# Performance work log

Hardware: AMD Instinct MI355X
Metric: run time of the kernel (lower is better)

## Reference

```python
import jax, jax.numpy as jnp
import numpy as np

C = 19
D = 128
TAU_HARD = 0.2
EMA = 0.999
BETA = 0.7
TH_I, TH_F = 0.5, 0.85
TL_I, TL_F = 0.1, 0.3
EPS = 1e-7


def _l2norm(x, axis):
    n = jnp.linalg.norm(x, axis=axis, keepdims=True)
    return x / jnp.maximum(n, 1e-12)


def _flatten_feat(feat):
    # [B,D,Hf,Wf] -> [N,D]
    B, Dd, Hf, Wf = feat.shape
    return feat.transpose(0, 2, 3, 1).reshape(-1, Dd)


def _build_protos(feat, labels, weights=None):
    # single-pass segment reduce replacing the per-class python loop
    f = _flatten_feat(feat)
    seg = labels.reshape(-1)
    w = jnp.ones(seg.shape, f.dtype) if weights is None else weights.reshape(-1)
    wsum_f = jax.ops.segment_sum(w[:, None] * f, seg, num_segments=C)  # [C,D]
    wsum = jax.ops.segment_sum(w, seg, num_segments=C)                 # [C]
    cnt = jax.ops.segment_sum(jnp.ones_like(w), seg, num_segments=C)
    proto = wsum_f / (wsum[:, None] + EPS)
    return proto, cnt >= 1.0


def _hard_contrastive(feat, labels, mem, mem_init):
    f = _l2norm(_flatten_feat(feat), axis=1)          # [N,D]
    lab = labels.reshape(-1)
    valid = mem_init[lab].astype(f.dtype)
    logits = (f @ mem.T) / TAU_HARD                   # [N,C]
    ce = -jnp.take_along_axis(jax.nn.log_softmax(logits, axis=1), lab[:, None], axis=1)[:, 0]
    nv = jnp.sum(valid)
    return jnp.where(nv > 0, jnp.sum(ce * valid) / jnp.maximum(nv, 1.0), 0.0)


def _ce_map(logits, target):
    # per-pixel cross entropy, logits [B,C,H,W], target [B,H,W]
    ls = jax.nn.log_softmax(logits, axis=1)
    return -jnp.take_along_axis(ls, target[:, None], axis=1)[:, 0]


def setup_inputs() -> dict:
    key = jax.random.key(0)
    ks = jax.random.split(key, 9)
    B, Hf, Wf = 4, 128, 128
    H = W = 512
    f = lambda k: jax.random.normal(k, (B, D, Hf, Wf), jnp.float32)
    g = lambda k: jax.random.normal(k, (B, C, H, W), jnp.float32)
    return {
        "feat_l1": f(ks[0]), "feat_l2": f(ks[1]),
        "feat_u1": f(ks[2]), "feat_u2": f(ks[3]),
        "logits_l1": g(ks[4]), "logits_l2": g(ks[5]),
        "logits_u1": g(ks[6]), "logits_u2": g(ks[7]),
        "memory": jnp.zeros((C, D), jnp.float32),
        "gt_labels": jax.random.randint(ks[8], (B, H, W), 0, C),
        "memory_init": jnp.zeros((C,), bool),
        "cur_iter": 10000,
        "max_iter": 40000,
    }


def reference(feat_l1, feat_l2, feat_u1, feat_u2, logits_l1, logits_l2,
              logits_u1, logits_u2, memory, gt_labels, memory_init,
              cur_iter, max_iter):
    B, _, Hf, Wf = feat_l1.shape
    H, W = logits_u1.shape[2], logits_u1.shape[3]

    q_u1 = jax.nn.softmax(logits_u1, axis=1)
    q_u2 = jax.nn.softmax(logits_u2, axis=1)

    # reliability r_u [B,H,W]
    y1 = jnp.argmax(q_u1, axis=1)
    y2 = jnp.argmax(q_u2, axis=1)
    agree = (y1 == y2).astype(q_u1.dtype)
    conf = (jnp.max(q_u1, axis=1) + jnp.max(q_u2, axis=1)) / 2.0
    m = (q_u1 + q_u2) / 2.0
    logm = jnp.log(jnp.maximum(m, EPS))
    kl1 = jnp.sum(q_u1 * (jnp.log(jnp.maximum(q_u1, EPS)) - logm), axis=1)
    kl2 = jnp.sum(q_u2 * (jnp.log(jnp.maximum(q_u2, EPS)) - logm), axis=1)
    r_u = agree * conf * jnp.exp(-(kl1 + kl2) / 2.0)

    # cosine-annealed thresholds
    ratio = float(cur_iter) / max(int(max_iter), 1)
    tau_high = TH_F - (TH_F - TH_I) * np.cos(np.pi * ratio / 2)

    # UCPS (pseudo labels are argmax of logits == argmax of softmax)
    loss_ucps = jnp.mean(jax.lax.stop_gradient(r_u) * (_ce_map(logits_u1, y2) + _ce_map(logits_u2, y1)))

    # nearest downsample (integer stride, matches torch nearest floor indexing)
    ih = jnp.arange(Hf) * (H // Hf)
    iw = jnp.arange(Wf) * (W // Wf)
    gt_down = gt_labels[:, ih][:, :, iw]
    pseudo_consensus = jnp.where(y1 != y2, 0, y1)
    pseudo_u_down = pseudo_consensus[:, ih][:, :, iw]
    # bilinear (align_corners=False == half-pixel, no antialias)
    r_u_down = jax.image.resize(r_u, (B, Hf, Wf), method='linear', antialias=False)

    anchor_mask = r_u_down > tau_high

    feat_l = (feat_l1 + feat_l2) / 2.0
    feat_u = (feat_u1 + feat_u2) / 2.0
    pl, pl_pres = _build_protos(feat_l, gt_down)
    anchor_r = jnp.where(anchor_mask, r_u_down, 0.0)
    pu, pu_pres = _build_protos(feat_u, pseudo_u_down, anchor_r)

    both = pl_pres & pu_pres
    merged = jnp.where(both[:, None], BETA * pl + (1.0 - BETA) * pu,
                       jnp.where(pl_pres[:, None], pl, pu))
    present = pl_pres | pu_pres
    merged = jax.lax.stop_gradient(merged)  # update_memory is no_grad

    p_norm = _l2norm(merged, axis=1)
    ema = _l2norm(EMA * memory + (1.0 - EMA) * p_norm, axis=1)
    new_mem = jnp.where((present & ~memory_init)[:, None], p_norm,
                        jnp.where((present & memory_init)[:, None], ema, memory))
    new_init = memory_init | present
    new_mem = jax.lax.stop_gradient(new_mem)

    loss_hard_l = (_hard_contrastive(feat_l1, gt_down, new_mem, new_init)
                   + _hard_contrastive(feat_l2, gt_down, new_mem, new_init)) / 2.0
    # contrastive_mode == 'all_hard'
    loss_hard_u = (_hard_contrastive(feat_u1, pseudo_u_down, new_mem, new_init)
                   + _hard_contrastive(feat_u2, pseudo_u_down, new_mem, new_init)) / 2.0

    loss_dgpc = loss_hard_l + loss_hard_u  # loss_soft == 0 in all_hard mode
    return jnp.stack([loss_dgpc, loss_ucps])
```

## Files before the change

kernel.cpp:

```cpp
#include <hip/hip_runtime.h>
#include <math.h>

#define NCLS 19
#define DD   128
#define EPSV 1e-7f
#define LOGEPS -16.118095651f

#define OFF_TAU    0
#define OFF_CNTL   8
#define OFF_WSUMU  32
#define OFF_CNTU   64
#define OFF_CE     96
#define OFF_VALID  100
#define OFF_UCPS   104
#define OFF_SUML   128
#define OFF_SUMU   2560
#define OFF_MEM    4992
#define OFF_INIT   7424
#define OFF_RUD    7456
#define OFF_PSEUDO 72992
#define ZERO_N     72992

__device__ __forceinline__ void fatom(float* p, float v) { unsafeAtomicAdd(p, v); }

__global__ __launch_bounds__(256) void kZ(float* __restrict__ W,
                                          const int* __restrict__ cur_it,
                                          const int* __restrict__ max_it) {
    int i = blockIdx.x * 256 + threadIdx.x;
    if (i == 0) {
        int mi = max_it[0]; if (mi < 1) mi = 1;
        double ratio = (double)cur_it[0] / (double)mi;
        W[OFF_TAU] = (float)(0.85 - (0.85 - 0.5) * cos(M_PI * ratio * 0.5));
    } else if (i < ZERO_N) {
        W[i] = 0.0f;
    }
}

__global__ __launch_bounds__(256, 2) void kB(const float* __restrict__ lu1,
                                             const float* __restrict__ lu2,
                                             float* __restrict__ W) {
    float* rud = W + OFF_RUD;
    int* pseudo = (int*)(W + OFF_PSEUDO);
    int t = blockIdx.x * 256 + threadIdx.x;
    int b = t >> 16;
    int rem4 = (t << 2) & 262143;
    int h = rem4 >> 9, w0 = rem4 & 511;

    const float4* p1 = (const float4*)lu1 + (size_t)b * (NCLS * 65536) + (rem4 >> 2);
    const float4* p2 = (const float4*)lu2 + (size_t)b * (NCLS * 65536) + (rem4 >> 2);

    float4 v1[NCLS], v2[NCLS];
#pragma unroll
    for (int c = 0; c < NCLS; c++) v1[c] = p1[c * 65536];
#pragma unroll
    for (int c = 0; c < NCLS; c++) v2[c] = p2[c * 65536];
    const float* a1 = (const float*)v1;
    const float* a2 = (const float*)v2;

    float contrib = 0.f;
    float ru12 = 0.f;
    int pl0 = 0;

#pragma unroll
    for (int e = 0; e < 4; e++) {
        float m1 = a1[e]; int y1 = 0;
        float m2 = a2[e]; int y2 = 0;
#pragma unroll
        for (int c = 1; c < NCLS; c++) {
            float x1 = a1[c * 4 + e], x2 = a2[c * 4 + e];
            if (x1 > m1) { m1 = x1; y1 = c; }
            if (x2 > m2) { m2 = x2; y2 = c; }
        }
        float s1 = 0.f, s2 = 0.f;
#pragma unroll
        for (int c = 0; c < NCLS; c++) {
            s1 += __expf(a1[c * 4 + e] - m1);
            s2 += __expf(a2[c * 4 + e] - m2);
        }
        float lse1 = m1 + __logf(s1);
        float lse2 = m2 + __logf(s2);

        float kl = 0.f, l1y2 = a1[e], l2y1 = a2[e];
#pragma unroll
        for (int c = 0; c < NCLS; c++) {
            float x1 = a1[c * 4 + e], x2 = a2[c * 4 + e];
            float lq1 = x1 - lse1, lq2 = x2 - lse2;
            float q1 = __expf(lq1), q2 = __expf(lq2);
            float mm = 0.5f * (q1 + q2);
            float lm = __logf(fmaxf(mm, EPSV));
            kl += q1 * (fmaxf(lq1, LOGEPS) - lm) + q2 * (fmaxf(lq2, LOGEPS) - lm);
            if (c == y2) l1y2 = x1;
            if (c == y1) l2y1 = x2;
        }
        float conf = 0.5f * (1.f / s1 + 1.f / s2);
        float r_u = (y1 == y2) ? conf * __expf(-0.5f * kl) : 0.f;
        float ce = (lse1 - l1y2) + (lse2 - l2y1);
        contrib += r_u * ce;
        if (e == 1 || e == 2) ru12 += r_u;
        if (e == 0) pl0 = (y1 == y2) ? y1 : 0;
    }

    float cs = contrib;
#pragma unroll
    for (int o = 32; o > 0; o >>= 1) cs += __shfl_down(cs, o, 64);
    __shared__ float wsum[4];
    if ((threadIdx.x & 63) == 0) wsum[threadIdx.x >> 6] = cs;
    __syncthreads();
    if (threadIdx.x == 0) fatom(&W[OFF_UCPS], wsum[0] + wsum[1] + wsum[2] + wsum[3]);

    int hm = h & 3;
    int didx = b * 16384 + (h >> 2) * 128 + (w0 >> 2);
    if (hm == 1 || hm == 2) fatom(&rud[didx], 0.25f * ru12);
    if (hm == 0) pseudo[didx] = pl0;
}

__global__ __launch_bounds__(256) void kC(const float* __restrict__ fl1,
                                          const float* __restrict__ fl2,
                                          const float* __restrict__ fu1,
                                          const float* __restrict__ fu2,
                                          const int* __restrict__ gt,
                                          float* __restrict__ W) {
    __shared__ float tile[DD * 33];
    __shared__ float accL[2 * NCLS * DD];
    __shared__ int   sLab[32], sCu[32];
    __shared__ float sW[32];
    __shared__ float sCntL[NCLS], sCntU[NCLS], sWUs[NCLS];

    int tid = threadIdx.x;
    for (int i = tid; i < 2 * NCLS * DD; i += 256) accL[i] = 0.f;
    if (tid < NCLS) { sCntL[tid] = 0.f; sCntU[tid] = 0.f; sWUs[tid] = 0.f; }
    __syncthreads();

    int P0 = blockIdx.x * 128;
    int b = P0 >> 14;
    const float tau = W[OFF_TAU];
    const float* rud = W + OFF_RUD;
    const int* pseudo = (const int*)(W + OFF_PSEUDO);
    size_t gb = (size_t)b * 2097152;

    int d = tid & 127, pg = tid >> 7;

    for (int T = 0; T < 4; T++) {
        int rem0 = (P0 + T * 32) & 16383;
        if (tid < 32) {
            int rem = rem0 + tid;
            int bp = b * 16384 + rem;
            int ii = rem >> 7, jj = rem & 127;
            int cl = gt[b * 262144 + ii * 2048 + jj * 4];
            int cu = pseudo[bp];
            float rd = rud[bp];
            float w = (rd > tau) ? rd : 0.f;
            sLab[tid] = cl; sCu[tid] = cu; sW[tid] = w;
            fatom(&sCntL[cl], 1.f);
            fatom(&sCntU[cu], 1.f);
            if (w > 0.f) fatom(&sWUs[cu], w);
        }
        for (int i = tid; i < 1024; i += 256) {
            int dd = i >> 3, p4 = (i & 7) << 2;
            size_t g = gb + (size_t)dd * 16384 + rem0 + p4;
            float4 x1 = *(const float4*)(fl1 + g);
            float4 x2 = *(const float4*)(fl2 + g);
            float* tp = &tile[dd * 33 + p4];
            tp[0] = 0.5f * (x1.x + x2.x);
            tp[1] = 0.5f * (x1.y + x2.y);
            tp[2] = 0.5f * (x1.z + x2.z);
            tp[3] = 0.5f * (x1.w + x2.w);
        }
        __syncthreads();
        float* aL = &accL[pg * (NCLS * DD) + d];
#pragma unroll
        for (int p = pg * 16; p < pg * 16 + 16; p++) {
            int c = sLab[p];
            aL[c * DD] += tile[d * 33 + p];
            float w = sW[p];
            if (w > 0.f) {
                size_t g = gb + (size_t)d * 16384 + rem0 + p;
                fatom(&W[OFF_SUMU + sCu[p] * DD + d], w * 0.5f * (fu1[g] + fu2[g]));
            }
        }
        __syncthreads();
    }
    for (int i = tid; i < NCLS * DD; i += 256)
        fatom(&W[OFF_SUML + i], accL[i] + accL[NCLS * DD + i]);
    if (tid < NCLS) {
        fatom(&W[OFF_CNTL + tid], sCntL[tid]);
        fatom(&W[OFF_WSUMU + tid], sWUs[tid]);
        fatom(&W[OFF_CNTU + tid], sCntU[tid]);
    }
}

__global__ __launch_bounds__(128) void kD(const float* __restrict__ mem,
                                          const unsigned char* __restrict__ minit,
                                          float* __restrict__ W) {
    int c = blockIdx.x, d = threadIdx.x;
    __shared__ float red[128];
    float cntL = W[OFF_CNTL + c], wsU = W[OFF_WSUMU + c], cntU = W[OFF_CNTU + c];
    bool plp = cntL >= 1.f, pup = cntU >= 1.f;
    float pl = W[OFF_SUML + c * DD + d] / (cntL + EPSV);
    float pu = W[OFF_SUMU + c * DD + d] / (wsU + EPSV);
    float merged = (plp && pup) ? (0.7f * pl + 0.3f * pu) : (plp ? pl : pu);

    red[d] = merged * merged; __syncthreads();
    for (int s = 64; s > 0; s >>= 1) { if (d < s) red[d] += red[d + s]; __syncthreads(); }
    float nrm = red[0];
    __syncthreads();
    float pn = merged / fmaxf(sqrtf(nrm), 1e-12f);

    float mo = mem[c * DD + d];
    float e = 0.999f * mo + 0.001f * pn;
    red[d] = e * e; __syncthreads();
    for (int s = 64; s > 0; s >>= 1) { if (d < s) red[d] += red[d + s]; __syncthreads(); }
    float ne = red[0];
    float ema = e / fmaxf(sqrtf(ne), 1e-12f);

    bool present = plp || pup;
    bool init = (minit[c] != 0);
    float nm = present ? (init ? ema : pn) : mo;
    W[OFF_MEM + c * DD + d] = nm;
    if (d == 0) W[OFF_INIT + c] = (init || present) ? 1.f : 0.f;
}

__device__ __forceinline__ void pix_loss(const float dots[NCLS], float nn, int lab,
                                         const float* sInit, float& ce_acc, float& v_acc) {
    float inv = 5.0f / fmaxf(sqrtf(nn), 1e-12f);
    float lg[NCLS];
#pragma unroll
    for (int c = 0; c < NCLS; c++) lg[c] = dots[c] * inv;
    float mx = lg[0];
#pragma unroll
    for (int c = 1; c < NCLS; c++) mx = fmaxf(mx, lg[c]);
    float s = 0.f;
#pragma unroll
    for (int c = 0; c < NCLS; c++) s += __expf(lg[c] - mx);
    float lse = mx + __logf(s);
    float ll = lg[0];
#pragma unroll
    for (int c = 1; c < NCLS; c++) if (c == lab) ll = lg[c];
    float vld = sInit[lab];
    ce_acc += vld * (lse - ll);
    v_acc += vld;
}

__global__ __launch_bounds__(256) void kE(const float* __restrict__ f0,
                                          const float* __restrict__ f1,
                                          const float* __restrict__ f2,
                                          const float* __restrict__ f3,
                                          const int* __restrict__ gt,
                                          float* __restrict__ W) {
    __shared__ __align__(16) float sMem[NCLS * DD];
    __shared__ float sInit[NCLS];
    __shared__ float redA[256], redB[256];
    int fid = blockIdx.y;
    const float* feat = (fid == 0) ? f0 : (fid == 1) ? f1 : (fid == 2) ? f2 : f3;
    for (int i = threadIdx.x; i < NCLS * DD; i += 256) sMem[i] = W[OFF_MEM + i];
    if (threadIdx.x < NCLS) sInit[threadIdx.x] = W[OFF_INIT + threadIdx.x];
    __syncthreads();

    int p0 = blockIdx.x * 512 + threadIdx.x;
    int b = p0 >> 14;
    int rem0 = p0 & 16383;
    const float* fp = feat + (size_t)b * 2097152 + rem0;

    float dots0[NCLS], dots1[NCLS];
#pragma unroll
    for (int c = 0; c < NCLS; c++) { dots0[c] = 0.f; dots1[c] = 0.f; }
    float n0 = 0.f, n1 = 0.f;

    for (int d0 = 0; d0 < DD; d0 += 8) {
        const float* fpp = fp + (size_t)d0 * 16384;
        float a[8], bb[8];
#pragma unroll
        for (int j = 0; j < 8; j++) {
            a[j]  = fpp[(size_t)j * 16384];
            bb[j] = fpp[(size_t)j * 16384 + 256];
        }
#pragma unroll
        for (int j = 0; j < 8; j++) { n0 += a[j] * a[j]; n1 += bb[j] * bb[j]; }
#pragma unroll
        for (int c = 0; c < NCLS; c++) {
            float4 m0 = *(const float4*)&sMem[c * DD + d0];
            float4 m1 = *(const float4*)&sMem[c * DD + d0 + 4];
            dots0[c] += a[0] * m0.x + a[1] * m0.y + a[2] * m0.z + a[3] * m0.w
                      + a[4] * m1.x + a[5] * m1.y + a[6] * m1.z + a[7] * m1.w;
            dots1[c] += bb[0] * m0.x + bb[1] * m0.y + bb[2] * m0.z + bb[3] * m0.w
                      + bb[4] * m1.x + bb[5] * m1.y + bb[6] * m1.z + bb[7] * m1.w;
        }
    }

    const int* pseudo = (const int*)(W + OFF_PSEUDO);
    int rem1 = rem0 + 256;
    int lab0 = (fid < 2) ? gt[b * 262144 + (rem0 >> 7) * 2048 + (rem0 & 127) * 4] : pseudo[p0];
    int lab1 = (fid < 2) ? gt[b * 262144 + (rem1 >> 7) * 2048 + (rem1 & 127) * 4] : pseudo[p0 + 256];

    float ce_acc = 0.f, v_acc = 0.f;
    pix_loss(dots0, n0, lab0, sInit, ce_acc, v_acc);
    pix_loss(dots1, n1, lab1, sInit, ce_acc, v_acc);

    redA[threadIdx.x] = ce_acc;
    redB[threadIdx.x] = v_acc;
    __syncthreads();
    for (int s = 128; s > 0; s >>= 1) {
        if (threadIdx.x < s) { redA[threadIdx.x] += redA[threadIdx.x + s]; redB[threadIdx.x] += redB[threadIdx.x + s]; }
        __syncthreads();
    }
    if (threadIdx.x == 0) {
        fatom(&W[OFF_CE + fid], redA[0]);
        fatom(&W[OFF_VALID + fid], redB[0]);
    }
}

__global__ void kF(float* __restrict__ out, const float* __restrict__ W) {
    if (threadIdx.x == 0 && blockIdx.x == 0) {
        float h[4];
#pragma unroll
        for (int i = 0; i < 4; i++) {
            float nv = W[OFF_VALID + i];
            h[i] = (nv > 0.f) ? W[OFF_CE + i] / fmaxf(nv, 1.f) : 0.f;
        }
        out[0] = 0.5f * (h[0] + h[1]) + 0.5f * (h[2] + h[3]);
        out[1] = W[OFF_UCPS] * (1.0f / 1048576.0f);
    }
}

extern "C" void kernel_launch(void* const* d_in, const int* in_sizes, int n_in,
                              void* d_out, int out_size, void* d_ws, size_t ws_size,
                              hipStream_t stream) {
    const float* fl1 = (const float*)d_in[0];
    const float* fl2 = (const float*)d_in[1];
    const float* fu1 = (const float*)d_in[2];
    const float* fu2 = (const float*)d_in[3];
    const float* lu1 = (const float*)d_in[6];
    const float* lu2 = (const float*)d_in[7];
    const float* mem = (const float*)d_in[8];
    const int* gt = (const int*)d_in[9];
    const unsigned char* minit = (const unsigned char*)d_in[10];
    const int* cur = (const int*)d_in[11];
    const int* mxi = (const int*)d_in[12];
    float* W = (float*)d_ws;
    float* out = (float*)d_out;

    kZ<<<286, 256, 0, stream>>>(W, cur, mxi);
    kB<<<1024, 256, 0, stream>>>(lu1, lu2, W);
    kC<<<512, 256, 0, stream>>>(fl1, fl2, fu1, fu2, gt, W);
    kD<<<NCLS, 128, 0, stream>>>(mem, minit, W);
    kE<<<dim3(128, 4), 256, 0, stream>>>(fl1, fl2, fu1, fu2, gt, W);
    kF<<<1, 64, 0, stream>>>(out, W);
}
```

Baseline: 419.2 us.

## Compute the KL and CE terms only for pixels where the two argmaxes agree

The pseudo-label kernel now runs an argmax-only first pass, one image row per block with float2 loads. Pixels whose two argmaxes agree are compacted into shared memory, and only those run the logsumexp, KL and CE work, reading their logits a second time. Pixels that disagree contribute zero weight, so their transcendental work is skipped exactly. In exchange, surviving pixels reload their logits with scattered scalar loads, and the kernel adds shared-memory atomics and higher occupancy launch bounds.

```diff
diff --git a/kernel.cpp b/kernel.cpp
--- a/kernel.cpp
+++ b/kernel.cpp
@@ -36,82 +36,103 @@
     }
 }
 
-__global__ __launch_bounds__(256, 2) void kB(const float* __restrict__ lu1,
+__global__ __launch_bounds__(256, 6) void kB(const float* __restrict__ lu1,
                                              const float* __restrict__ lu2,
                                              float* __restrict__ W) {
+    __shared__ unsigned int sPk[512];
+    __shared__ float sM1[512], sM2[512];
+    __shared__ unsigned int sCnt;
+    __shared__ float sCE;
+
     float* rud = W + OFF_RUD;
     int* pseudo = (int*)(W + OFF_PSEUDO);
-    int t = blockIdx.x * 256 + threadIdx.x;
-    int b = t >> 16;
-    int rem4 = (t << 2) & 262143;
-    int h = rem4 >> 9, w0 = rem4 & 511;
-
-    const float4* p1 = (const float4*)lu1 + (size_t)b * (NCLS * 65536) + (rem4 >> 2);
-    const float4* p2 = (const float4*)lu2 + (size_t)b * (NCLS * 65536) + (rem4 >> 2);
-
-    float4 v1[NCLS], v2[NCLS];
-#pragma unroll
-    for (int c = 0; c < NCLS; c++) v1[c] = p1[c * 65536];
-#pragma unroll
-    for (int c = 0; c < NCLS; c++) v2[c] = p2[c * 65536];
-    const float* a1 = (const float*)v1;
-    const float* a2 = (const float*)v2;
-
-    float contrib = 0.f;
-    float ru12 = 0.f;
-    int pl0 = 0;
-
-#pragma unroll
-    for (int e = 0; e < 4; e++) {
-        float m1 = a1[e]; int y1 = 0;
-        float m2 = a2[e]; int y2 = 0;
-#pragma unroll
-        for (int c = 1; c < NCLS; c++) {
-            float x1 = a1[c * 4 + e], x2 = a2[c * 4 + e];
-            if (x1 > m1) { m1 = x1; y1 = c; }
-            if (x2 > m2) { m2 = x2; y2 = c; }
-        }
-        float s1 = 0.f, s2 = 0.f;
+
+    int blk = blockIdx.x;
+    int b = blk >> 9;
+    int h = blk & 511;
+    int t = threadIdx.x;
+    if (t == 0) { sCnt = 0u; sCE = 0.f; }
+    __syncthreads();
+
+    size_t base = (size_t)b * (NCLS * 262144) + (size_t)h * 512;
+    const float2* p1 = (const float2*)(lu1 + base) + t;
+    const float2* p2 = (const float2*)(lu2 + base) + t;
+
+    float m1a, m1b, m2a, m2b;
+    int y1a = 0, y1b = 0, y2a = 0, y2b = 0;
+    {
+        float2 x1 = p1[0], x2 = p2[0];
+        m1a = x1.x; m1b = x1.y; m2a = x2.x; m2b = x2.y;
+    }
+#pragma unroll
+    for (int c = 1; c < NCLS; c++) {
+        float2 x1 = p1[(size_t)c * 131072];
+        float2 x2 = p2[(size_t)c * 131072];
+        if (x1.x > m1a) { m1a = x1.x; y1a = c; }
+        if (x1.y > m1b) { m1b = x1.y; y1b = c; }
+        if (x2.x > m2a) { m2a = x2.x; y2a = c; }
+        if (x2.y > m2b) { m2b = x2.y; y2b = c; }
+    }
+
+    int wa = t << 1, wb = wa + 1;
+    bool aga = (y1a == y2a), agb = (y1b == y2b);
+
+    if ((h & 3) == 0 && (t & 1) == 0)
+        pseudo[b * 16384 + (h >> 2) * 128 + (wa >> 2)] = aga ? y1a : 0;
+
+    if (aga) {
+        unsigned int i = atomicAdd(&sCnt, 1u);
+        sPk[i] = ((unsigned)wa << 5) | (unsigned)y1a;
+        sM1[i] = m1a; sM2[i] = m2a;
+    }
+    if (agb) {
+        unsigned int i = atomicAdd(&sCnt, 1u);
+        sPk[i] = ((unsigned)wb << 5) | (unsigned)y1b;
+        sM1[i] = m1b; sM2[i] = m2b;
+    }
+    __syncthreads();
+
+    int n = (int)sCnt;
+    int hm = h & 3;
+    for (int i = t; i < n; i += 256) {
+        unsigned pk = sPk[i];
+        int w = (int)(pk >> 5), y = (int)(pk & 31u);
+        float m1 = sM1[i], m2 = sM2[i];
+        const float* q1 = lu1 + base + w;
+        const float* q2 = lu2 + base + w;
+
+        float s1 = 0.f, s2 = 0.f, l1y = 0.f, l2y = 0.f;
 #pragma unroll
         for (int c = 0; c < NCLS; c++) {
-            s1 += __expf(a1[c * 4 + e] - m1);
-            s2 += __expf(a2[c * 4 + e] - m2);
+            float x1 = q1[(size_t)c * 262144];
+            float x2 = q2[(size_t)c * 262144];
+            s1 += __expf(x1 - m1);
+            s2 += __expf(x2 - m2);
+            if (c == y) { l1y = x1; l2y = x2; }
         }
         float lse1 = m1 + __logf(s1);
         float lse2 = m2 + __logf(s2);
 
-        float kl = 0.f, l1y2 = a1[e], l2y1 = a2[e];
+        float kl = 0.f;
 #pragma unroll
         for (int c = 0; c < NCLS; c++) {
-            float x1 = a1[c * 4 + e], x2 = a2[c * 4 + e];
+            float x1 = q1[(size_t)c * 262144];
+            float x2 = q2[(size_t)c * 262144];
             float lq1 = x1 - lse1, lq2 = x2 - lse2;
-            float q1 = __expf(lq1), q2 = __expf(lq2);
-            float mm = 0.5f * (q1 + q2);
+            float e1 = __expf(lq1), e2 = __expf(lq2);
+            float mm = 0.5f * (e1 + e2);
             float lm = __logf(fmaxf(mm, EPSV));
-            kl += q1 * (fmaxf(lq1, LOGEPS) - lm) + q2 * (fmaxf(lq2, LOGEPS) - lm);
-            if (c == y2) l1y2 = x1;
-            if (c == y1) l2y1 = x2;
+            kl += e1 * (fmaxf(lq1, LOGEPS) - lm) + e2 * (fmaxf(lq2, LOGEPS) - lm);
         }
         float conf = 0.5f * (1.f / s1 + 1.f / s2);
-        float r_u = (y1 == y2) ? conf * __expf(-0.5f * kl) : 0.f;
-        float ce = (lse1 - l1y2) + (lse2 - l2y1);
-        contrib += r_u * ce;
-        if (e == 1 || e == 2) ru12 += r_u;
-        if (e == 0) pl0 = (y1 == y2) ? y1 : 0;
-    }
-
-    float cs = contrib;
-#pragma unroll
-    for (int o = 32; o > 0; o >>= 1) cs += __shfl_down(cs, o, 64);
-    __shared__ float wsum[4];
-    if ((threadIdx.x & 63) == 0) wsum[threadIdx.x >> 6] = cs;
-    __syncthreads();
-    if (threadIdx.x == 0) fatom(&W[OFF_UCPS], wsum[0] + wsum[1] + wsum[2] + wsum[3]);
-
-    int hm = h & 3;
-    int didx = b * 16384 + (h >> 2) * 128 + (w0 >> 2);
-    if (hm == 1 || hm == 2) fatom(&rud[didx], 0.25f * ru12);
-    if (hm == 0) pseudo[didx] = pl0;
+        float r_u = conf * __expf(-0.5f * kl);
+        float ce = (lse1 - l1y) + (lse2 - l2y);
+        fatom(&sCE, r_u * ce);
+        if ((hm == 1 || hm == 2) && ((w & 3) == 1 || (w & 3) == 2))
+            fatom(&rud[b * 16384 + (h >> 2) * 128 + (w >> 2)], 0.25f * r_u);
+    }
+    __syncthreads();
+    if (t == 0) fatom(&W[OFF_UCPS], sCE);
 }
 
 __global__ __launch_bounds__(256) void kC(const float* __restrict__ fl1,
@@ -340,7 +361,7 @@
     float* out = (float*)d_out;
 
     kZ<<<286, 256, 0, stream>>>(W, cur, mxi);
-    kB<<<1024, 256, 0, stream>>>(lu1, lu2, W);
+    kB<<<2048, 256, 0, stream>>>(lu1, lu2, W);
     kC<<<512, 256, 0, stream>>>(fl1, fl2, fu1, fu2, gt, W);
     kD<<<NCLS, 128, 0, stream>>>(mem, minit, W);
     kE<<<dim3(128, 4), 256, 0, stream>>>(fl1, fl2, fu1, fu2, gt, W);
```

After: 435.9 us. 4.0% more time.
